# Performance work log

Hardware: AMD Instinct MI355X
Metric: run time of the kernel (lower is better)

Reference implementation:

```python
import jax, jax.numpy as jnp
import numpy as np

N_NODES = 10000
N_EDGES = 320000
D = 256
D_OUT = 256
NUM_REL = 2


def setup_inputs() -> dict:
    key = jax.random.key(0)
    ks = jax.random.split(key, 16)
    s = 1.0 / np.sqrt(D)
    inp = {}
    inp['feat'] = jax.random.normal(ks[0], (N_NODES, D), dtype=jnp.float32)
    inp['src'] = jax.random.randint(ks[1], (N_EDGES,), 0, N_NODES, dtype=jnp.int32)
    inp['dst'] = jax.random.randint(ks[2], (N_EDGES,), 0, N_NODES, dtype=jnp.int32)
    inp['rel'] = jax.random.randint(ks[3], (N_EDGES,), 0, NUM_REL, dtype=jnp.int32)
    # per-relation edgeNN: ONE tied Linear(D, D) applied twice with relu
    inp['W_rel'] = jax.random.normal(ks[4], (NUM_REL, D, D), dtype=jnp.float32) * s
    inp['b_rel'] = jax.random.normal(ks[5], (NUM_REL, D), dtype=jnp.float32) * s
    # LSTM (single step from zero state: W_hh contributes 0, omitted)
    inp['W_ih'] = jax.random.normal(ks[6], (4 * D, D), dtype=jnp.float32) * s
    inp['b_ih'] = jax.random.normal(ks[7], (4 * D,), dtype=jnp.float32) * s
    inp['b_hh'] = jax.random.normal(ks[8], (4 * D,), dtype=jnp.float32) * s
    # global_update MLP: D -> D/2 -> D/2 -> D_OUT
    h = D // 2
    inp['W1'] = jax.random.normal(ks[9], (h, D), dtype=jnp.float32) * s
    inp['b1'] = jax.random.normal(ks[10], (h,), dtype=jnp.float32) * s
    inp['W2'] = jax.random.normal(ks[11], (h, h), dtype=jnp.float32) * (1.0 / np.sqrt(h))
    inp['b2'] = jax.random.normal(ks[12], (h,), dtype=jnp.float32) * (1.0 / np.sqrt(h))
    inp['W3'] = jax.random.normal(ks[13], (D_OUT, h), dtype=jnp.float32) * (1.0 / np.sqrt(h))
    inp['b3'] = jax.random.normal(ks[14], (D_OUT,), dtype=jnp.float32) * (1.0 / np.sqrt(h))
    return inp


def reference(feat, src, dst, rel, W_rel, b_rel, W_ih, b_ih, b_hh,
              W1, b1, W2, b2, W3, b3):
    n_nodes = feat.shape[0]
    # ---- message: per-edge relation-typed tied-weight MLP ----
    S = feat[src]  # [E, D] gather of source features

    def edge_nn(x, W, b):
        h = jax.nn.relu(x @ W.T + b)
        return jax.nn.relu(h @ W.T + b)  # same lin1 applied twice (tied)

    msgs = jnp.zeros_like(S)
    for r in range(W_rel.shape[0]):  # small fixed relation count
        msgs = jnp.where((rel == r)[:, None], edge_nn(S, W_rel[r], b_rel[r]), msgs)

    # ---- reduce: scatter-sum into destination nodes ----
    agg = jax.ops.segment_sum(msgs, dst, num_segments=n_nodes)  # [N, D]

    # ---- apply: per-node single-step LSTM from zero (h0, c0) ----
    gates = agg @ W_ih.T + b_ih + b_hh  # [N, 4D], torch gate order i,f,g,o
    i, f, g, o = jnp.split(gates, 4, axis=-1)
    c = jax.nn.sigmoid(i) * jnp.tanh(g)  # f * c0 = 0
    hn = jax.nn.sigmoid(o) * jnp.tanh(c)  # [N, D]

    # ---- global_update MLP ----
    x = jax.nn.relu(hn @ W1.T + b1)
    x = jax.nn.relu(x @ W2.T + b2)
    return x @ W3.T + b3  # [N, D_OUT]
```

## Files before the change

kernel.cpp:

```cpp
#include <hip/hip_runtime.h>
#include <hip/hip_bf16.h>

#define N_NODES 10000
#define N_EDGES 320000
#define D 256

typedef __attribute__((ext_vector_type(8))) _Float16 f16x8;
typedef __attribute__((ext_vector_type(4))) _Float16 f16x4;
typedef __attribute__((ext_vector_type(4))) float f32x4;

__device__ __forceinline__ void async_copy16(const void* g, void* l) {
  __builtin_amdgcn_global_load_lds(
      (const __attribute__((address_space(1))) unsigned int*)g,
      (__attribute__((address_space(3))) unsigned int*)l, 16, 0, 0);
}

template<int ROWS, int WAVES>
__device__ __forceinline__ void stage_tile(const _Float16* __restrict__ Wb, int k0, int K,
                                           _Float16* Bs, int wave, int lane) {
  const int sr = lane >> 2, ss = lane & 3;
#pragma unroll
  for (int grp = wave; grp < ROWS / 16; grp += WAVES) {
    int r = grp * 16 + sr;
    int gq = ss ^ ((r >> 1) & 3);
    async_copy16(Wb + (size_t)r * K + k0 + gq * 8, Bs + grp * 512);
  }
}
__device__ __forceinline__ f16x8 read_B(const _Float16* Bs, int r, int quad) {
  return *(const f16x8*)(Bs + r * 32 + (quad ^ ((r >> 1) & 3)) * 8);
}

__device__ __forceinline__ f16x8 load_B(const _Float16* __restrict__ W, int row, int K,
                                        int kc, int quad) {
  return *(const f16x8*)(W + (size_t)row * K + kc * 32 + quad * 8);
}

__device__ __forceinline__ float fast_sigmoid(float x) {
  return __builtin_amdgcn_rcpf(1.f + __expf(-x));
}
__device__ __forceinline__ float fast_tanh(float x) {
  float ax = fabsf(x);
  float e = __expf(-2.f * ax);
  float t = (1.f - e) * __builtin_amdgcn_rcpf(1.f + e);
  return copysignf(t, x);
}

__global__ __launch_bounds__(512) void prep_cast(
    int* __restrict__ cnt,
    const float* __restrict__ W_rel, const float* __restrict__ W_ih,
    const float* __restrict__ b_ih, const float* __restrict__ b_hh,
    const float* __restrict__ W1, const float* __restrict__ W2,
    const float* __restrict__ W3,
    _Float16* __restrict__ W_relh, _Float16* __restrict__ Wg,
    float* __restrict__ bg,
    _Float16* __restrict__ W1h, _Float16* __restrict__ W2h,
    _Float16* __restrict__ W3h) {
  int i = blockIdx.x * 512 + threadIdx.x;
  if (i < 10240) { if (i < N_NODES) cnt[i] = 0; return; }
  i -= 10240;
  if (i < 131072) { W_relh[i] = (_Float16)W_rel[i]; return; }
  i -= 131072;
  if (i < 196608) {
    int p = i >> 8, k = i & 255;
    int t = p / 48, rem = p - t * 48;
    int phase = rem >> 4, u = rem & 15;
    int orig = t * 16 + u + (phase == 1 ? 512 : (phase == 2 ? 768 : 0));
    Wg[i] = (_Float16)W_ih[orig * 256 + k]; return;
  }
  i -= 196608;
  if (i < 32768) { W1h[i] = (_Float16)W1[i]; return; }
  i -= 32768;
  if (i < 16384) { W2h[i] = (_Float16)W2[i]; return; }
  i -= 16384;
  if (i < 32768) { W3h[i] = (_Float16)W3[i]; return; }
  i -= 32768;
  if (i < 768) {
    int t = i / 48, rem = i - t * 48;
    int phase = rem >> 4, u = rem & 15;
    int orig = t * 16 + u + (phase == 1 ? 512 : (phase == 2 ? 768 : 0));
    bg[i] = b_ih[orig] + b_hh[orig];
  }
}

__global__ __launch_bounds__(512) void edge_fill(
    const float* __restrict__ feat, const _Float16* __restrict__ W_relh,
    const float* __restrict__ b_rel, _Float16* __restrict__ Mh,
    const int* __restrict__ dst, const int* __restrict__ src,
    const int* __restrict__ rel,
    int* __restrict__ cnt, unsigned int* __restrict__ rowoff)
{
  __shared__ _Float16 Hs[64 * 266];
  __shared__ alignas(16) _Float16 Bs[256 * 32];
  const int b = blockIdx.x;
  if (b >= 314) {
    int i = (b - 314) * 512 + threadIdx.x;
    int v = dst[i];
    int pos = atomicAdd(&cnt[v], 1);
    if (pos < 128)
      rowoff[(v << 7) + pos] = (unsigned int)((rel[i] * N_NODES + src[i]) * D);
    return;
  }
  const int t = threadIdx.x;
  const int wave = t >> 6, lane = t & 63;
  const int quad = lane >> 4, lrow = lane & 15;
  const int z = (b >= 157) ? 1 : 0;
  const int m0 = (b - z * 157) * 64;
  const _Float16* Wb = W_relh + z * 65536;
  const float* bb = b_rel + z * 256;
  const int wm = (wave >> 2) * 32;
  const int wn = (wave & 3) * 64;

  int ar0 = m0 + wm + lrow;      if (ar0 > N_NODES - 1) ar0 = N_NODES - 1;
  int ar1 = m0 + wm + 16 + lrow; if (ar1 > N_NODES - 1) ar1 = N_NODES - 1;
  const float* fr0 = feat + (size_t)ar0 * 256;
  const float* fr1 = feat + (size_t)ar1 * 256;

  f32x4 acc[2][4];
#pragma unroll
  for (int i = 0; i < 2; ++i)
#pragma unroll
    for (int j = 0; j < 4; ++j) acc[i][j] = (f32x4)0.0f;

#pragma unroll
  for (int kc = 0; kc < 8; ++kc) {
    stage_tile<256, 8>(Wb, kc * 32, 256, Bs, wave, lane);
    float4 u0 = *(const float4*)(fr0 + kc * 32 + quad * 8);
    float4 u1 = *(const float4*)(fr0 + kc * 32 + quad * 8 + 4);
    float4 v0 = *(const float4*)(fr1 + kc * 32 + quad * 8);
    float4 v1 = *(const float4*)(fr1 + kc * 32 + quad * 8 + 4);
    f16x8 af0, af1;
    af0[0] = (_Float16)u0.x; af0[1] = (_Float16)u0.y; af0[2] = (_Float16)u0.z; af0[3] = (_Float16)u0.w;
    af0[4] = (_Float16)u1.x; af0[5] = (_Float16)u1.y; af0[6] = (_Float16)u1.z; af0[7] = (_Float16)u1.w;
    af1[0] = (_Float16)v0.x; af1[1] = (_Float16)v0.y; af1[2] = (_Float16)v0.z; af1[3] = (_Float16)v0.w;
    af1[4] = (_Float16)v1.x; af1[5] = (_Float16)v1.y; af1[6] = (_Float16)v1.z; af1[7] = (_Float16)v1.w;
    __syncthreads();
#pragma unroll
    for (int j = 0; j < 4; ++j) {
      f16x8 bf = read_B(Bs, wn + j * 16 + lrow, quad);
      acc[0][j] = __builtin_amdgcn_mfma_f32_16x16x32_f16(af0, bf, acc[0][j], 0, 0, 0);
      acc[1][j] = __builtin_amdgcn_mfma_f32_16x16x32_f16(af1, bf, acc[1][j], 0, 0, 0);
    }
    __syncthreads();
  }
#pragma unroll
  for (int i = 0; i < 2; ++i) {
    int rb = wm + i * 16 + quad * 4;
#pragma unroll
    for (int j = 0; j < 4; ++j) {
      int col = wn + j * 16 + lrow;
      float bv = bb[col];
#pragma unroll
      for (int reg = 0; reg < 4; ++reg) {
        Hs[(rb + reg) * 266 + col] = (_Float16)fmaxf(acc[i][j][reg] + bv, 0.f);
        acc[i][j][reg] = 0.f;
      }
    }
  }
  __syncthreads();

#pragma unroll
  for (int kc = 0; kc < 8; ++kc) {
    stage_tile<256, 8>(Wb, kc * 32, 256, Bs, wave, lane);
    f16x8 af0 = *(const f16x8*)(Hs + (wm + lrow) * 266 + kc * 32 + quad * 8);
    f16x8 af1 = *(const f16x8*)(Hs + (wm + 16 + lrow) * 266 + kc * 32 + quad * 8);
    __syncthreads();
#pragma unroll
    for (int j = 0; j < 4; ++j) {
      f16x8 bf = read_B(Bs, wn + j * 16 + lrow, quad);
      acc[0][j] = __builtin_amdgcn_mfma_f32_16x16x32_f16(af0, bf, acc[0][j], 0, 0, 0);
      acc[1][j] = __builtin_amdgcn_mfma_f32_16x16x32_f16(af1, bf, acc[1][j], 0, 0, 0);
    }
    __syncthreads();
  }
  _Float16* Mo = Mh + (size_t)z * (N_NODES * D);
#pragma unroll
  for (int i = 0; i < 2; ++i) {
    int rb = m0 + wm + i * 16 + quad * 4;
#pragma unroll
    for (int j = 0; j < 4; ++j) {
      int col = wn + j * 16 + lrow;
      float bv = bb[col];
#pragma unroll
      for (int reg = 0; reg < 4; ++reg) {
        int gm = rb + reg;
        if (gm < N_NODES)
          Mo[(size_t)gm * D + col] = (_Float16)fmaxf(acc[i][j][reg] + bv, 0.f);
      }
    }
  }
}

__global__ __launch_bounds__(256) void agg_kernel(const int* __restrict__ cnt,
                                                  const unsigned int* __restrict__ rowoff,
                                                  const _Float16* __restrict__ Mh,
                                                  _Float16* __restrict__ aggh) {
  __shared__ float part[4][256];
  const int node = blockIdx.x;
  const int wave = threadIdx.x >> 6, lane = threadIdx.x & 63;
  const int base = node << 7;
  const int deg = cnt[node];
  float a0 = 0.f, a1 = 0.f, a2 = 0.f, a3 = 0.f;
  for (int j = wave; j < deg; j += 4) {
    unsigned int off = rowoff[base + j];
    f16x4 v = *(const f16x4*)(Mh + (size_t)off + lane * 4);
    a0 += (float)v[0]; a1 += (float)v[1]; a2 += (float)v[2]; a3 += (float)v[3];
  }
  *(float4*)&part[wave][lane * 4] = make_float4(a0, a1, a2, a3);
  __syncthreads();
  if (wave == 0) {
    float4 p0 = *(const float4*)&part[0][lane * 4];
    float4 p1 = *(const float4*)&part[1][lane * 4];
    float4 p2 = *(const float4*)&part[2][lane * 4];
    float4 p3 = *(const float4*)&part[3][lane * 4];
    f16x4 o;
    o[0] = (_Float16)(p0.x + p1.x + p2.x + p3.x);
    o[1] = (_Float16)(p0.y + p1.y + p2.y + p3.y);
    o[2] = (_Float16)(p0.z + p1.z + p2.z + p3.z);
    o[3] = (_Float16)(p0.w + p1.w + p2.w + p3.w);
    *(f16x4*)(aggh + (size_t)node * D + lane * 4) = o;
  }
}

__global__ __launch_bounds__(512) void tail(
    const _Float16* __restrict__ aggh,
    const _Float16* __restrict__ Wg, const float* __restrict__ bg,
    const _Float16* __restrict__ W1h, const float* __restrict__ b1,
    const _Float16* __restrict__ W2h, const float* __restrict__ b2,
    const _Float16* __restrict__ W3h, const float* __restrict__ b3,
    float* __restrict__ out)
{
  __shared__ _Float16 Hn[64 * 266];
  __shared__ _Float16 Xs[64 * 138];
  __shared__ _Float16 X2s[64 * 138];
  const int t = threadIdx.x;
  const int wave = t >> 6, lane = t & 63;
  const int quad = lane >> 4, lrow = lane & 15;
  const int r0 = blockIdx.x * 64;

  int ar[4];
#pragma unroll
  for (int m = 0; m < 4; ++m) {
    int a = r0 + m * 16 + lrow;
    ar[m] = (a > N_NODES - 1) ? (N_NODES - 1) : a;
  }

  {
    f32x4 acc[4][6];
#pragma unroll
    for (int m = 0; m < 4; ++m)
#pragma unroll
      for (int j = 0; j < 6; ++j) acc[m][j] = (f32x4)0.0f;

    f16x8 afp[2][4], bfp[2][6];
#pragma unroll
    for (int m = 0; m < 4; ++m)
      afp[0][m] = *(const f16x8*)(aggh + (size_t)ar[m] * 256 + quad * 8);
#pragma unroll
    for (int j = 0; j < 6; ++j)
      bfp[0][j] = load_B(Wg, (wave * 6 + j) * 16 + lrow, 256, 0, quad);

#pragma unroll
    for (int kc = 0; kc < 8; ++kc) {
      const int cur = kc & 1, nxt = cur ^ 1;
      if (kc < 7) {
#pragma unroll
        for (int m = 0; m < 4; ++m)
          afp[nxt][m] = *(const f16x8*)(aggh + (size_t)ar[m] * 256 + (kc + 1) * 32 + quad * 8);
#pragma unroll
        for (int j = 0; j < 6; ++j)
          bfp[nxt][j] = load_B(Wg, (wave * 6 + j) * 16 + lrow, 256, kc + 1, quad);
      }
#pragma unroll
      for (int j = 0; j < 6; ++j)
#pragma unroll
        for (int m = 0; m < 4; ++m)
          acc[m][j] = __builtin_amdgcn_mfma_f32_16x16x32_f16(afp[cur][m], bfp[cur][j], acc[m][j], 0, 0, 0);
    }
#pragma unroll
    for (int m = 0; m < 4; ++m) {
#pragma unroll
      for (int p = 0; p < 2; ++p) {
        float bvi = bg[(wave * 6 + 3 * p + 0) * 16 + lrow];
        float bvg = bg[(wave * 6 + 3 * p + 1) * 16 + lrow];
        float bvo = bg[(wave * 6 + 3 * p + 2) * 16 + lrow];
        int dcol = (wave * 2 + p) * 16 + lrow;
#pragma unroll
        for (int reg = 0; reg < 4; ++reg) {
          float vi = acc[m][3 * p + 0][reg] + bvi;
          float vg = acc[m][3 * p + 1][reg] + bvg;
          float vo = acc[m][3 * p + 2][reg] + bvo;
          float c = fast_sigmoid(vi) * fast_tanh(vg);
          Hn[(m * 16 + quad * 4 + reg) * 266 + dcol] = (_Float16)(fast_sigmoid(vo) * fast_tanh(c));
        }
      }
    }
  }
  __syncthreads();

  {
    f32x4 acc[4];
#pragma unroll
    for (int m = 0; m < 4; ++m) acc[m] = (f32x4)0.0f;
    f16x8 bfp[2];
    bfp[0] = load_B(W1h, wave * 16 + lrow, 256, 0, quad);
#pragma unroll
    for (int kc = 0; kc < 8; ++kc) {
      const int cur = kc & 1, nxt = cur ^ 1;
      if (kc < 7) bfp[nxt] = load_B(W1h, wave * 16 + lrow, 256, kc + 1, quad);
#pragma unroll
      for (int m = 0; m < 4; ++m) {
        f16x8 a = *(const f16x8*)(Hn + (m * 16 + lrow) * 266 + kc * 32 + quad * 8);
        acc[m] = __builtin_amdgcn_mfma_f32_16x16x32_f16(a, bfp[cur], acc[m], 0, 0, 0);
      }
    }
    int col = wave * 16 + lrow;
    float bv = b1[col];
#pragma unroll
    for (int m = 0; m < 4; ++m)
#pragma unroll
      for (int reg = 0; reg < 4; ++reg)
        Xs[(m * 16 + quad * 4 + reg) * 138 + col] = (_Float16)fmaxf(acc[m][reg] + bv, 0.f);
  }
  __syncthreads();

  {
    f32x4 acc[4];
#pragma unroll
    for (int m = 0; m < 4; ++m) acc[m] = (f32x4)0.0f;
    f16x8 bfp[2];
    bfp[0] = load_B(W2h, wave * 16 + lrow, 128, 0, quad);
#pragma unroll
    for (int kc = 0; kc < 4; ++kc) {
      const int cur = kc & 1, nxt = cur ^ 1;
      if (kc < 3) bfp[nxt] = load_B(W2h, wave * 16 + lrow, 128, kc + 1, quad);
#pragma unroll
      for (int m = 0; m < 4; ++m) {
        f16x8 a = *(const f16x8*)(Xs + (m * 16 + lrow) * 138 + kc * 32 + quad * 8);
        acc[m] = __builtin_amdgcn_mfma_f32_16x16x32_f16(a, bfp[cur], acc[m], 0, 0, 0);
      }
    }
    int col = wave * 16 + lrow;
    float bv = b2[col];
#pragma unroll
    for (int m = 0; m < 4; ++m)
#pragma unroll
      for (int reg = 0; reg < 4; ++reg)
        X2s[(m * 16 + quad * 4 + reg) * 138 + col] = (_Float16)fmaxf(acc[m][reg] + bv, 0.f);
  }
  __syncthreads();

  {
    f32x4 acc[4][2];
#pragma unroll
    for (int m = 0; m < 4; ++m) { acc[m][0] = (f32x4)0.0f; acc[m][1] = (f32x4)0.0f; }
    f16x8 bfp[2][2];
#pragma unroll
    for (int j = 0; j < 2; ++j)
      bfp[0][j] = load_B(W3h, wave * 32 + j * 16 + lrow, 128, 0, quad);
#pragma unroll
    for (int kc = 0; kc < 4; ++kc) {
      const int cur = kc & 1, nxt = cur ^ 1;
      if (kc < 3) {
#pragma unroll
        for (int j = 0; j < 2; ++j)
          bfp[nxt][j] = load_B(W3h, wave * 32 + j * 16 + lrow, 128, kc + 1, quad);
      }
#pragma unroll
      for (int m = 0; m < 4; ++m) {
        f16x8 a = *(const f16x8*)(X2s + (m * 16 + lrow) * 138 + kc * 32 + quad * 8);
#pragma unroll
        for (int j = 0; j < 2; ++j)
          acc[m][j] = __builtin_amdgcn_mfma_f32_16x16x32_f16(a, bfp[cur][j], acc[m][j], 0, 0, 0);
      }
    }
#pragma unroll
    for (int m = 0; m < 4; ++m) {
#pragma unroll
      for (int j = 0; j < 2; ++j) {
        int col = wave * 32 + j * 16 + lrow;
        float bv = b3[col];
#pragma unroll
        for (int reg = 0; reg < 4; ++reg) {
          int gm = r0 + m * 16 + quad * 4 + reg;
          if (gm < N_NODES)
            out[(size_t)gm * 256 + col] = acc[m][j][reg] + bv;
        }
      }
    }
  }
}

extern "C" void kernel_launch(void* const* d_in, const int* in_sizes, int n_in,
                              void* d_out, int out_size, void* d_ws, size_t ws_size,
                              hipStream_t stream) {
  const float* feat  = (const float*)d_in[0];
  const int* src = (const int*)d_in[1];
  const int* dst = (const int*)d_in[2];
  const int* rel = (const int*)d_in[3];
  const float* W_rel = (const float*)d_in[4];
  const float* b_rel = (const float*)d_in[5];
  const float* W_ih  = (const float*)d_in[6];
  const float* b_ih  = (const float*)d_in[7];
  const float* b_hh  = (const float*)d_in[8];
  const float* W1 = (const float*)d_in[9];
  const float* b1 = (const float*)d_in[10];
  const float* W2 = (const float*)d_in[11];
  const float* b2 = (const float*)d_in[12];
  const float* W3 = (const float*)d_in[13];
  const float* b3 = (const float*)d_in[14];
  float* out = (float*)d_out;

  char* ws = (char*)d_ws;
  _Float16* Mh   = (_Float16*)(ws);
  _Float16* aggh = (_Float16*)(ws + 10240000);
  char* wsb = ws + 15360000;
  _Float16* W_relh = (_Float16*)(wsb);
  _Float16* Wg     = (_Float16*)(wsb + 262144);
  _Float16* W1h    = (_Float16*)(wsb + 655360);
  _Float16* W2h    = (_Float16*)(wsb + 720896);
  _Float16* W3h    = (_Float16*)(wsb + 753664);
  float*    bg     = (float*)(wsb + 819200);
  int*      cnt    = (int*)(wsb + 822272);
  unsigned int* rowoff = (unsigned int*)(wsb + 862272);

  prep_cast<<<822, 512, 0, stream>>>(cnt, W_rel, W_ih, b_ih, b_hh, W1, W2, W3,
                                     W_relh, Wg, bg, W1h, W2h, W3h);
  edge_fill<<<939, 512, 0, stream>>>(feat, W_relh, b_rel, Mh,
                                     dst, src, rel, cnt, rowoff);
  agg_kernel<<<N_NODES, 256, 0, stream>>>(cnt, rowoff, Mh, aggh);
  tail<<<157, 512, 0, stream>>>(aggh, Wg, bg, W1h, b1, W2h, b2, W3h, b3, out);
}
```

Baseline: 192.3 us.

## Restructure edge GEMM to 4-wave blocks loading weights directly with register prefetch

The per-relation node MLP kernel moves from 8 waves to 4 waves per block, each wave now covering all 64 rows by 64 columns. Weight tiles are read straight from global memory into registers with a double-buffered prefetch, replacing the LDS staging and its two barriers per k-chunk. This removes the barrier and LDS-traffic costs and overlaps loads with MFMA work. In exchange it uses more registers and repeats global/L2 weight reads in every wave. The edge-bucketing blocks are resized to 256 threads, and the grid size is adjusted to match.

```diff
diff --git a/kernel.cpp b/kernel.cpp
--- a/kernel.cpp
+++ b/kernel.cpp
@@ -9,30 +9,18 @@
 typedef __attribute__((ext_vector_type(4))) _Float16 f16x4;
 typedef __attribute__((ext_vector_type(4))) float f32x4;
 
-__device__ __forceinline__ void async_copy16(const void* g, void* l) {
-  __builtin_amdgcn_global_load_lds(
-      (const __attribute__((address_space(1))) unsigned int*)g,
-      (__attribute__((address_space(3))) unsigned int*)l, 16, 0, 0);
-}
-
-template<int ROWS, int WAVES>
-__device__ __forceinline__ void stage_tile(const _Float16* __restrict__ Wb, int k0, int K,
-                                           _Float16* Bs, int wave, int lane) {
-  const int sr = lane >> 2, ss = lane & 3;
-#pragma unroll
-  for (int grp = wave; grp < ROWS / 16; grp += WAVES) {
-    int r = grp * 16 + sr;
-    int gq = ss ^ ((r >> 1) & 3);
-    async_copy16(Wb + (size_t)r * K + k0 + gq * 8, Bs + grp * 512);
-  }
-}
-__device__ __forceinline__ f16x8 read_B(const _Float16* Bs, int r, int quad) {
-  return *(const f16x8*)(Bs + r * 32 + (quad ^ ((r >> 1) & 3)) * 8);
-}
-
 __device__ __forceinline__ f16x8 load_B(const _Float16* __restrict__ W, int row, int K,
                                         int kc, int quad) {
   return *(const f16x8*)(W + (size_t)row * K + kc * 32 + quad * 8);
+}
+
+__device__ __forceinline__ f16x8 load_A_f32(const float* __restrict__ fr, int kc, int quad) {
+  float4 u0 = *(const float4*)(fr + kc * 32 + quad * 8);
+  float4 u1 = *(const float4*)(fr + kc * 32 + quad * 8 + 4);
+  f16x8 af;
+  af[0] = (_Float16)u0.x; af[1] = (_Float16)u0.y; af[2] = (_Float16)u0.z; af[3] = (_Float16)u0.w;
+  af[4] = (_Float16)u1.x; af[5] = (_Float16)u1.y; af[6] = (_Float16)u1.z; af[7] = (_Float16)u1.w;
+  return af;
 }
 
 __device__ __forceinline__ float fast_sigmoid(float x) {
@@ -82,7 +70,8 @@
   }
 }
 
-__global__ __launch_bounds__(512) void edge_fill(
+#define NB_GEMM 314
+__global__ __launch_bounds__(256) void edge_fill(
     const float* __restrict__ feat, const _Float16* __restrict__ W_relh,
     const float* __restrict__ b_rel, _Float16* __restrict__ Mh,
     const int* __restrict__ dst, const int* __restrict__ src,
@@ -90,10 +79,9 @@
     int* __restrict__ cnt, unsigned int* __restrict__ rowoff)
 {
   __shared__ _Float16 Hs[64 * 266];
-  __shared__ alignas(16) _Float16 Bs[256 * 32];
   const int b = blockIdx.x;
-  if (b >= 314) {
-    int i = (b - 314) * 512 + threadIdx.x;
+  if (b >= NB_GEMM) {
+    int i = (b - NB_GEMM) * 256 + threadIdx.x;
     int v = dst[i];
     int pos = atomicAdd(&cnt[v], 1);
     if (pos < 128)
@@ -107,75 +95,84 @@
   const int m0 = (b - z * 157) * 64;
   const _Float16* Wb = W_relh + z * 65536;
   const float* bb = b_rel + z * 256;
-  const int wm = (wave >> 2) * 32;
-  const int wn = (wave & 3) * 64;
-
-  int ar0 = m0 + wm + lrow;      if (ar0 > N_NODES - 1) ar0 = N_NODES - 1;
-  int ar1 = m0 + wm + 16 + lrow; if (ar1 > N_NODES - 1) ar1 = N_NODES - 1;
-  const float* fr0 = feat + (size_t)ar0 * 256;
-  const float* fr1 = feat + (size_t)ar1 * 256;
-
-  f32x4 acc[2][4];
-#pragma unroll
-  for (int i = 0; i < 2; ++i)
-#pragma unroll
-    for (int j = 0; j < 4; ++j) acc[i][j] = (f32x4)0.0f;
-
-#pragma unroll
-  for (int kc = 0; kc < 8; ++kc) {
-    stage_tile<256, 8>(Wb, kc * 32, 256, Bs, wave, lane);
-    float4 u0 = *(const float4*)(fr0 + kc * 32 + quad * 8);
-    float4 u1 = *(const float4*)(fr0 + kc * 32 + quad * 8 + 4);
-    float4 v0 = *(const float4*)(fr1 + kc * 32 + quad * 8);
-    float4 v1 = *(const float4*)(fr1 + kc * 32 + quad * 8 + 4);
-    f16x8 af0, af1;
-    af0[0] = (_Float16)u0.x; af0[1] = (_Float16)u0.y; af0[2] = (_Float16)u0.z; af0[3] = (_Float16)u0.w;
-    af0[4] = (_Float16)u1.x; af0[5] = (_Float16)u1.y; af0[6] = (_Float16)u1.z; af0[7] = (_Float16)u1.w;
-    af1[0] = (_Float16)v0.x; af1[1] = (_Float16)v0.y; af1[2] = (_Float16)v0.z; af1[3] = (_Float16)v0.w;
-    af1[4] = (_Float16)v1.x; af1[5] = (_Float16)v1.y; af1[6] = (_Float16)v1.z; af1[7] = (_Float16)v1.w;
-    __syncthreads();
-#pragma unroll
-    for (int j = 0; j < 4; ++j) {
-      f16x8 bf = read_B(Bs, wn + j * 16 + lrow, quad);
-      acc[0][j] = __builtin_amdgcn_mfma_f32_16x16x32_f16(af0, bf, acc[0][j], 0, 0, 0);
-      acc[1][j] = __builtin_amdgcn_mfma_f32_16x16x32_f16(af1, bf, acc[1][j], 0, 0, 0);
-    }
-    __syncthreads();
-  }
-#pragma unroll
-  for (int i = 0; i < 2; ++i) {
-    int rb = wm + i * 16 + quad * 4;
+  const int wn = wave * 64;
+
+  const float* fr[4];
+#pragma unroll
+  for (int m = 0; m < 4; ++m) {
+    int a = m0 + m * 16 + lrow;
+    if (a > N_NODES - 1) a = N_NODES - 1;
+    fr[m] = feat + (size_t)a * 256;
+  }
+
+  f32x4 acc[4][4];
+#pragma unroll
+  for (int m = 0; m < 4; ++m)
+#pragma unroll
+    for (int j = 0; j < 4; ++j) acc[m][j] = (f32x4)0.0f;
+
+  {
+    f16x8 afp[2][4], bfp[2][4];
+#pragma unroll
+    for (int m = 0; m < 4; ++m) afp[0][m] = load_A_f32(fr[m], 0, quad);
+#pragma unroll
+    for (int j = 0; j < 4; ++j) bfp[0][j] = load_B(Wb, wn + j * 16 + lrow, 256, 0, quad);
+#pragma unroll
+    for (int kc = 0; kc < 8; ++kc) {
+      const int cur = kc & 1, nxt = cur ^ 1;
+      if (kc < 7) {
+#pragma unroll
+        for (int m = 0; m < 4; ++m) afp[nxt][m] = load_A_f32(fr[m], kc + 1, quad);
+#pragma unroll
+        for (int j = 0; j < 4; ++j) bfp[nxt][j] = load_B(Wb, wn + j * 16 + lrow, 256, kc + 1, quad);
+      }
+#pragma unroll
+      for (int j = 0; j < 4; ++j)
+#pragma unroll
+        for (int m = 0; m < 4; ++m)
+          acc[m][j] = __builtin_amdgcn_mfma_f32_16x16x32_f16(afp[cur][m], bfp[cur][j], acc[m][j], 0, 0, 0);
+    }
+  }
+#pragma unroll
+  for (int m = 0; m < 4; ++m) {
+    int rb = m * 16 + quad * 4;
 #pragma unroll
     for (int j = 0; j < 4; ++j) {
       int col = wn + j * 16 + lrow;
       float bv = bb[col];
 #pragma unroll
       for (int reg = 0; reg < 4; ++reg) {
-        Hs[(rb + reg) * 266 + col] = (_Float16)fmaxf(acc[i][j][reg] + bv, 0.f);
-        acc[i][j][reg] = 0.f;
+        Hs[(rb + reg) * 266 + col] = (_Float16)fmaxf(acc[m][j][reg] + bv, 0.f);
+        acc[m][j][reg] = 0.f;
       }
     }
   }
   __syncthreads();
 
-#pragma unroll
-  for (int kc = 0; kc < 8; ++kc) {
-    stage_tile<256, 8>(Wb, kc * 32, 256, Bs, wave, lane);
-    f16x8 af0 = *(const f16x8*)(Hs + (wm + lrow) * 266 + kc * 32 + quad * 8);
-    f16x8 af1 = *(const f16x8*)(Hs + (wm + 16 + lrow) * 266 + kc * 32 + quad * 8);
-    __syncthreads();
-#pragma unroll
-    for (int j = 0; j < 4; ++j) {
-      f16x8 bf = read_B(Bs, wn + j * 16 + lrow, quad);
-      acc[0][j] = __builtin_amdgcn_mfma_f32_16x16x32_f16(af0, bf, acc[0][j], 0, 0, 0);
-      acc[1][j] = __builtin_amdgcn_mfma_f32_16x16x32_f16(af1, bf, acc[1][j], 0, 0, 0);
-    }
-    __syncthreads();
+  {
+    f16x8 bfp[2][4];
+#pragma unroll
+    for (int j = 0; j < 4; ++j) bfp[0][j] = load_B(Wb, wn + j * 16 + lrow, 256, 0, quad);
+#pragma unroll
+    for (int kc = 0; kc < 8; ++kc) {
+      const int cur = kc & 1, nxt = cur ^ 1;
+      if (kc < 7) {
+#pragma unroll
+        for (int j = 0; j < 4; ++j) bfp[nxt][j] = load_B(Wb, wn + j * 16 + lrow, 256, kc + 1, quad);
+      }
+#pragma unroll
+      for (int m = 0; m < 4; ++m) {
+        f16x8 a = *(const f16x8*)(Hs + (m * 16 + lrow) * 266 + kc * 32 + quad * 8);
+#pragma unroll
+        for (int j = 0; j < 4; ++j)
+          acc[m][j] = __builtin_amdgcn_mfma_f32_16x16x32_f16(a, bfp[cur][j], acc[m][j], 0, 0, 0);
+      }
+    }
   }
   _Float16* Mo = Mh + (size_t)z * (N_NODES * D);
 #pragma unroll
-  for (int i = 0; i < 2; ++i) {
-    int rb = m0 + wm + i * 16 + quad * 4;
+  for (int m = 0; m < 4; ++m) {
+    int rb = m0 + m * 16 + quad * 4;
 #pragma unroll
     for (int j = 0; j < 4; ++j) {
       int col = wn + j * 16 + lrow;
@@ -184,7 +181,7 @@
       for (int reg = 0; reg < 4; ++reg) {
         int gm = rb + reg;
         if (gm < N_NODES)
-          Mo[(size_t)gm * D + col] = (_Float16)fmaxf(acc[i][j][reg] + bv, 0.f);
+          Mo[(size_t)gm * D + col] = (_Float16)fmaxf(acc[m][j][reg] + bv, 0.f);
       }
     }
   }
@@ -425,8 +422,8 @@
 
   prep_cast<<<822, 512, 0, stream>>>(cnt, W_rel, W_ih, b_ih, b_hh, W1, W2, W3,
                                      W_relh, Wg, bg, W1h, W2h, W3h);
-  edge_fill<<<939, 512, 0, stream>>>(feat, W_relh, b_rel, Mh,
-                                     dst, src, rel, cnt, rowoff);
+  edge_fill<<<1564, 256, 0, stream>>>(feat, W_relh, b_rel, Mh,
+                                      dst, src, rel, cnt, rowoff);
   agg_kernel<<<N_NODES, 256, 0, stream>>>(cnt, rowoff, Mh, aggh);
   tail<<<157, 512, 0, stream>>>(aggh, Wg, bg, W1h, b1, W2h, b2, W3h, b3, out);
 }
```

After: 196.0 us. Within noise of the previous version (+1.9%).
